# Kernel tuning notes

Hardware: AMD Instinct MI355X
Metric: run time of the kernel (lower is better)

## Reference

```python
import jax, jax.numpy as jnp
from jax import lax
import numpy as np

B, T, F, H = 4096, 512, 8, 16  # batch, seq, n_features, hidden_dim


def _lstm(x, Wih, Whh, bih, bhh):
    """PyTorch-convention LSTM over batch-first x [B,T,in].
    Returns (h_T [B,H], outputs [B,T,H]). Gate order: i, f, g, o."""
    Bn = x.shape[0]
    Hn = Whh.shape[1]
    xs = jnp.swapaxes(x, 0, 1)                       # [T,B,in]
    x_proj = xs @ Wih.T + (bih + bhh)                # precompute input GEMM: [T,B,4H]

    def step(carry, xp):
        h, c = carry
        gates = xp + h @ Whh.T                       # [B,4H]
        i, f, g, o = jnp.split(gates, 4, axis=-1)
        i = jax.nn.sigmoid(i)
        f = jax.nn.sigmoid(f)
        g = jnp.tanh(g)
        o = jax.nn.sigmoid(o)
        c = f * c + i * g
        h = o * jnp.tanh(c)
        return (h, c), h

    h0 = jnp.zeros((Bn, Hn), x.dtype)
    (hT, _), hs = lax.scan(step, (h0, h0), x_proj)
    return hT, jnp.swapaxes(hs, 0, 1)                # [B,H], [B,T,H]


def setup_inputs() -> dict:
    key = jax.random.key(0)
    ks = jax.random.split(key, 11)
    s_e = 1.0 / np.sqrt(H)
    u = lambda k, shp: jax.random.uniform(k, shp, jnp.float32, -s_e, s_e)
    return {
        "x": jax.random.normal(ks[0], (B, T, F), jnp.float32),
        "enc_Wih": u(ks[1], (4 * H, F)),
        "enc_Whh": u(ks[2], (4 * H, H)),
        "enc_bih": u(ks[3], (4 * H,)),
        "enc_bhh": u(ks[4], (4 * H,)),
        "dec_Wih": u(ks[5], (4 * H, H)),
        "dec_Whh": u(ks[6], (4 * H, H)),
        "dec_bih": u(ks[7], (4 * H,)),
        "dec_bhh": u(ks[8], (4 * H,)),
        "out_W": u(ks[9], (F, H)),
        "out_b": u(ks[10], (F,)),
    }


def reference(x, enc_Wih, enc_Whh, enc_bih, enc_bhh,
              dec_Wih, dec_Whh, dec_bih, dec_bhh, out_W, out_b):
    # encoder: keep only final hidden state h_T
    hT, _ = _lstm(x, enc_Wih, enc_Whh, enc_bih, enc_bhh)   # [B,H]
    # repeat over time: h.squeeze(0).unsqueeze(1).repeat(1,T,1)
    repeated = jnp.broadcast_to(hT[:, None, :], (x.shape[0], x.shape[1], hT.shape[1]))
    _, decoded = _lstm(repeated, dec_Wih, dec_Whh, dec_bih, dec_bhh)  # [B,T,H]
    return decoded @ out_W.T + out_b                       # [B,T,F]
```

## Files before the change

### kernel.cpp

```cpp
#include <hip/hip_runtime.h>

#define B_ 4096
#define T_ 512
#define F_ 8
#define H_ 16

typedef float f32x2 __attribute__((ext_vector_type(2)));
typedef float f32x4v __attribute__((ext_vector_type(4)));

__device__ __forceinline__ f32x2 pkfma(f32x2 a, f32x2 b, f32x2 c) {
    return __builtin_elementwise_fma(a, b, c);
}
#define SV2(v, a, b) __builtin_shufflevector(v, v, a, b)

#define LOG2E 1.442695041f
#define N2LOG2E (-2.885390082f)

__device__ __forceinline__ float sigf(float x) {
    return __builtin_amdgcn_rcpf(1.0f + __builtin_amdgcn_exp2f(-LOG2E * x));
}
__device__ __forceinline__ float tanh_f(float x) {
    return __builtin_fmaf(2.0f,
        __builtin_amdgcn_rcpf(1.0f + __builtin_amdgcn_exp2f(N2LOG2E * x)), -1.0f);
}

__global__ __launch_bounds__(256, 1) void lstm_ae_kernel(
    const float* __restrict__ x,
    const float* __restrict__ eWih, const float* __restrict__ eWhh,
    const float* __restrict__ ebih, const float* __restrict__ ebhh,
    const float* __restrict__ dWih, const float* __restrict__ dWhh,
    const float* __restrict__ dbih, const float* __restrict__ dbhh,
    const float* __restrict__ oW,   const float* __restrict__ ob,
    float* __restrict__ out)
{
    const int tid = threadIdx.x;
    const int wv  = tid >> 6;
    const int l   = tid & 63;
    const int cw  = l >> 4;
    const int u   = l & 15;
    const int bw  = blockIdx.x * 16 + wv * 4;
    const int b   = bw + cw;

    __shared__ __align__(16) f32x2 hsh[4][40];
    __shared__ __align__(16) f32x2 xsh[4][4][33][4];

    const f32x2 zero2 = {0.0f, 0.0f};

    f32x2 wh[4][8], wi[4][4];
    float bias[4];
#pragma unroll
    for (int g = 0; g < 4; ++g) {
        const int r = g * 16 + u;
        const f32x2* phh = (const f32x2*)(eWhh + r * 16);
#pragma unroll
        for (int p = 0; p < 8; ++p) wh[g][p] = phh[p];
        const f32x2* pih = (const f32x2*)(eWih + r * 8);
#pragma unroll
        for (int p = 0; p < 4; ++p) wi[g][p] = pih[p];
        bias[g] = ebih[r] + ebhh[r];
    }

    float c = 0.0f;
    f32x2 hb[8];
#pragma unroll
    for (int p = 0; p < 8; ++p) hb[p] = zero2;

    float* hp = (float*)&hsh[wv][cw * 10];

    const int ps = l >> 1, phx = l & 1;
    f32x4v xr[4];
#pragma unroll
    for (int i = 0; i < 4; ++i)
        xr[i] = *(const f32x4v*)(x + ((size_t)(bw + i) * T_ + ps) * F_ + phx * 4);

    for (int c0 = 0; c0 < T_; c0 += 32) {
        __builtin_amdgcn_wave_barrier();
#pragma unroll
        for (int i = 0; i < 4; ++i)
            *(f32x4v*)&xsh[wv][i][ps][phx * 2] = xr[i];
        __builtin_amdgcn_wave_barrier();
        if (c0 + 32 < T_) {
#pragma unroll
            for (int i = 0; i < 4; ++i)
                xr[i] = *(const f32x4v*)(
                    x + ((size_t)(bw + i) * T_ + (c0 + 32 + ps)) * F_ + phx * 4);
        }
        for (int s = 0; s < 32; ++s) {
            f32x4v xq0 = *(const f32x4v*)&xsh[wv][cw][s][0];
            f32x4v xq1 = *(const f32x4v*)&xsh[wv][cw][s][2];
            f32x2 x0 = SV2(xq0, 0, 1), x1 = SV2(xq0, 2, 3);
            f32x2 x2 = SV2(xq1, 0, 1), x3 = SV2(xq1, 2, 3);

            f32x2 acc[4];
#pragma unroll
            for (int g = 0; g < 4; ++g) {
                f32x2 a = pkfma(wi[g][0], x0, f32x2{bias[g], 0.0f});
                a = pkfma(wi[g][1], x1, a);
                a = pkfma(wi[g][2], x2, a);
                a = pkfma(wi[g][3], x3, a);
#pragma unroll
                for (int p = 0; p < 8; ++p) a = pkfma(wh[g][p], hb[p], a);
                acc[g] = a;
            }
            const float gi = sigf(acc[0].x + acc[0].y);
            const float gf = sigf(acc[1].x + acc[1].y);
            const float gg = tanh_f(acc[2].x + acc[2].y);
            const float go = sigf(acc[3].x + acc[3].y);
            c = __builtin_fmaf(gf, c, gi * gg);
            const float ht = go * tanh_f(c);

            __builtin_amdgcn_wave_barrier();
            hp[u] = ht;
            __builtin_amdgcn_wave_barrier();
            f32x4v h0 = *(const f32x4v*)&hp[0];
            f32x4v h1 = *(const f32x4v*)&hp[4];
            f32x4v h2 = *(const f32x4v*)&hp[8];
            f32x4v h3 = *(const f32x4v*)&hp[12];
            hb[0] = SV2(h0, 0, 1); hb[1] = SV2(h0, 2, 3);
            hb[2] = SV2(h1, 0, 1); hb[3] = SV2(h1, 2, 3);
            hb[4] = SV2(h2, 0, 1); hb[5] = SV2(h2, 2, 3);
            hb[6] = SV2(h3, 0, 1); hb[7] = SV2(h3, 2, 3);
        }
    }

    f32x2 wd[4][8];
    float xp[4];
#pragma unroll
    for (int g = 0; g < 4; ++g) {
        const int r = g * 16 + u;
        const f32x2* pih = (const f32x2*)(dWih + r * 16);
        f32x2 a = zero2;
#pragma unroll
        for (int p = 0; p < 8; ++p) a = pkfma(pih[p], hb[p], a);
        xp[g] = dbih[r] + dbhh[r] + a.x + a.y;
        const f32x2* phh = (const f32x2*)(dWhh + r * 16);
#pragma unroll
        for (int p = 0; p < 8; ++p) wd[g][p] = phh[p];
    }
    f32x2 wo[8];
    {
        const f32x2* po = (const f32x2*)(oW + (u & 7) * 16);
#pragma unroll
        for (int p = 0; p < 8; ++p) wo[p] = po[p];
    }
    const float obv = ob[u & 7];
    const bool st = (u < 8);
    float* outp = out + (size_t)b * (T_ * F_);

    c = 0.0f;
#pragma unroll
    for (int p = 0; p < 8; ++p) hb[p] = zero2;

    for (int t = 0; t < T_; ++t) {
        f32x2 acc[4];
#pragma unroll
        for (int g = 0; g < 4; ++g) {
            f32x2 a = pkfma(wd[g][0], hb[0], f32x2{xp[g], 0.0f});
#pragma unroll
            for (int p = 1; p < 8; ++p) a = pkfma(wd[g][p], hb[p], a);
            acc[g] = a;
        }
        const float gi = sigf(acc[0].x + acc[0].y);
        const float gf = sigf(acc[1].x + acc[1].y);
        const float gg = tanh_f(acc[2].x + acc[2].y);
        const float go = sigf(acc[3].x + acc[3].y);
        c = __builtin_fmaf(gf, c, gi * gg);
        const float ht = go * tanh_f(c);

        __builtin_amdgcn_wave_barrier();
        hp[u] = ht;
        __builtin_amdgcn_wave_barrier();
        f32x4v h0 = *(const f32x4v*)&hp[0];
        f32x4v h1 = *(const f32x4v*)&hp[4];
        f32x4v h2 = *(const f32x4v*)&hp[8];
        f32x4v h3 = *(const f32x4v*)&hp[12];
        hb[0] = SV2(h0, 0, 1); hb[1] = SV2(h0, 2, 3);
        hb[2] = SV2(h1, 0, 1); hb[3] = SV2(h1, 2, 3);
        hb[4] = SV2(h2, 0, 1); hb[5] = SV2(h2, 2, 3);
        hb[6] = SV2(h3, 0, 1); hb[7] = SV2(h3, 2, 3);

        f32x2 oa = pkfma(wo[0], hb[0], f32x2{obv, 0.0f});
#pragma unroll
        for (int p = 1; p < 8; ++p) oa = pkfma(wo[p], hb[p], oa);
        if (st) outp[t * F_ + u] = oa.x + oa.y;
    }
}

extern "C" void kernel_launch(void* const* d_in, const int* in_sizes, int n_in,
                              void* d_out, int out_size, void* d_ws, size_t ws_size,
                              hipStream_t stream) {
    (void)in_sizes; (void)n_in; (void)d_ws; (void)ws_size; (void)out_size;
    lstm_ae_kernel<<<dim3(B_ / 16), dim3(256), 0, stream>>>(
        (const float*)d_in[0],
        (const float*)d_in[1], (const float*)d_in[2],
        (const float*)d_in[3], (const float*)d_in[4],
        (const float*)d_in[5], (const float*)d_in[6],
        (const float*)d_in[7], (const float*)d_in[8],
        (const float*)d_in[9], (const float*)d_in[10],
        (float*)d_out);
}
```

Measured before the change: 353.9 us.

## Split LSTM gates across 32 lanes per sequence with swizzle exchange

Moves from 16 lanes per batch element (each computing all four gates) to 32 lanes per element, each computing two gate rows. Gate activations are exchanged with ds_swizzle, and the output projection is split across lanes and reduced with swizzles. This halves the per-lane serial FMA chain on each recurrent step and doubles the grid, with launch bounds raised to allow two blocks per CU. The cost is twice as many lanes per sequence, extra cross-lane swizzles, and idle half-lanes during the h store.

```diff
diff --git a/kernel.cpp b/kernel.cpp
--- a/kernel.cpp
+++ b/kernel.cpp
@@ -23,8 +23,15 @@
     return __builtin_fmaf(2.0f,
         __builtin_amdgcn_rcpf(1.0f + __builtin_amdgcn_exp2f(N2LOG2E * x)), -1.0f);
 }
-
-__global__ __launch_bounds__(256, 1) void lstm_ae_kernel(
+template <int PAT>
+__device__ __forceinline__ float swz(float v) {
+    return __builtin_bit_cast(float,
+        __builtin_amdgcn_ds_swizzle(__builtin_bit_cast(int, v), PAT));
+}
+#define XOR8  0x201F
+#define XOR16 0x401F
+
+__global__ __launch_bounds__(256, 2) void lstm_ae_kernel(
     const float* __restrict__ x,
     const float* __restrict__ eWih, const float* __restrict__ eWhh,
     const float* __restrict__ ebih, const float* __restrict__ ebhh,
@@ -36,82 +43,89 @@
     const int tid = threadIdx.x;
     const int wv  = tid >> 6;
     const int l   = tid & 63;
-    const int cw  = l >> 4;
-    const int u   = l & 15;
-    const int bw  = blockIdx.x * 16 + wv * 4;
-    const int b   = bw + cw;
-
-    __shared__ __align__(16) f32x2 hsh[4][40];
-    __shared__ __align__(16) f32x2 xsh[4][4][33][4];
-
+    const int cw  = l >> 5;
+    const int w   = l & 31;
+    const int u   = w & 15;
+    const bool loh = (w < 16);
+    const int r0  = w;
+    const int r1  = w + 32;
+    const int b   = blockIdx.x * 8 + wv * 2 + cw;
+
+    __shared__ __align__(16) float hsh[4][2][16];
+    __shared__ __align__(16) float xsh[4][2][32][8];
+
+    const float ns1 = loh ? N2LOG2E : -LOG2E;
+    const float m1  = loh ? 2.0f : 1.0f;
+    const float c1  = loh ? -1.0f : 0.0f;
     const f32x2 zero2 = {0.0f, 0.0f};
 
-    f32x2 wh[4][8], wi[4][4];
-    float bias[4];
-#pragma unroll
-    for (int g = 0; g < 4; ++g) {
-        const int r = g * 16 + u;
-        const f32x2* phh = (const f32x2*)(eWhh + r * 16);
-#pragma unroll
-        for (int p = 0; p < 8; ++p) wh[g][p] = phh[p];
-        const f32x2* pih = (const f32x2*)(eWih + r * 8);
-#pragma unroll
-        for (int p = 0; p < 4; ++p) wi[g][p] = pih[p];
-        bias[g] = ebih[r] + ebhh[r];
-    }
+    f32x2 wh0[8], wh1[8], wi0[4], wi1[4];
+    {
+        const f32x2* p0 = (const f32x2*)(eWhh + r0 * 16);
+        const f32x2* p1 = (const f32x2*)(eWhh + r1 * 16);
+#pragma unroll
+        for (int p = 0; p < 8; ++p) { wh0[p] = p0[p]; wh1[p] = p1[p]; }
+        const f32x2* q0 = (const f32x2*)(eWih + r0 * 8);
+        const f32x2* q1 = (const f32x2*)(eWih + r1 * 8);
+#pragma unroll
+        for (int p = 0; p < 4; ++p) { wi0[p] = q0[p]; wi1[p] = q1[p]; }
+    }
+    const float bias0 = ebih[r0] + ebhh[r0];
+    const float bias1 = ebih[r1] + ebhh[r1];
 
     float c = 0.0f;
     f32x2 hb[8];
 #pragma unroll
     for (int p = 0; p < 8; ++p) hb[p] = zero2;
 
-    float* hp = (float*)&hsh[wv][cw * 10];
-
-    const int ps = l >> 1, phx = l & 1;
-    f32x4v xr[4];
-#pragma unroll
-    for (int i = 0; i < 4; ++i)
-        xr[i] = *(const f32x4v*)(x + ((size_t)(bw + i) * T_ + ps) * F_ + phx * 4);
+    const int sA = w >> 1, hA = (w & 1) * 4;
+    const float* xbase = x + (size_t)b * (T_ * F_);
+    f32x4v xrA = *(const f32x4v*)(xbase + sA * F_ + hA);
+    f32x4v xrB = *(const f32x4v*)(xbase + (sA + 16) * F_ + hA);
 
     for (int c0 = 0; c0 < T_; c0 += 32) {
         __builtin_amdgcn_wave_barrier();
-#pragma unroll
-        for (int i = 0; i < 4; ++i)
-            *(f32x4v*)&xsh[wv][i][ps][phx * 2] = xr[i];
+        *(f32x4v*)&xsh[wv][cw][sA][hA]      = xrA;
+        *(f32x4v*)&xsh[wv][cw][sA + 16][hA] = xrB;
         __builtin_amdgcn_wave_barrier();
         if (c0 + 32 < T_) {
-#pragma unroll
-            for (int i = 0; i < 4; ++i)
-                xr[i] = *(const f32x4v*)(
-                    x + ((size_t)(bw + i) * T_ + (c0 + 32 + ps)) * F_ + phx * 4);
+            xrA = *(const f32x4v*)(xbase + (c0 + 32 + sA) * F_ + hA);
+            xrB = *(const f32x4v*)(xbase + (c0 + 48 + sA) * F_ + hA);
         }
         for (int s = 0; s < 32; ++s) {
             f32x4v xq0 = *(const f32x4v*)&xsh[wv][cw][s][0];
-            f32x4v xq1 = *(const f32x4v*)&xsh[wv][cw][s][2];
+            f32x4v xq1 = *(const f32x4v*)&xsh[wv][cw][s][4];
             f32x2 x0 = SV2(xq0, 0, 1), x1 = SV2(xq0, 2, 3);
             f32x2 x2 = SV2(xq1, 0, 1), x3 = SV2(xq1, 2, 3);
 
-            f32x2 acc[4];
-#pragma unroll
-            for (int g = 0; g < 4; ++g) {
-                f32x2 a = pkfma(wi[g][0], x0, f32x2{bias[g], 0.0f});
-                a = pkfma(wi[g][1], x1, a);
-                a = pkfma(wi[g][2], x2, a);
-                a = pkfma(wi[g][3], x3, a);
-#pragma unroll
-                for (int p = 0; p < 8; ++p) a = pkfma(wh[g][p], hb[p], a);
-                acc[g] = a;
+            f32x2 aa0 = pkfma(wi0[0], x0, f32x2{bias0, 0.0f});
+            f32x2 ab0 = pkfma(wi0[1], x1, zero2);
+            f32x2 aa1 = pkfma(wi1[0], x0, f32x2{bias1, 0.0f});
+            f32x2 ab1 = pkfma(wi1[1], x1, zero2);
+            aa0 = pkfma(wi0[2], x2, aa0); ab0 = pkfma(wi0[3], x3, ab0);
+            aa1 = pkfma(wi1[2], x2, aa1); ab1 = pkfma(wi1[3], x3, ab1);
+#pragma unroll
+            for (int p = 0; p < 8; p += 2) {
+                aa0 = pkfma(wh0[p],   hb[p],   aa0);
+                ab0 = pkfma(wh0[p+1], hb[p+1], ab0);
+                aa1 = pkfma(wh1[p],   hb[p],   aa1);
+                ab1 = pkfma(wh1[p+1], hb[p+1], ab1);
             }
-            const float gi = sigf(acc[0].x + acc[0].y);
-            const float gf = sigf(acc[1].x + acc[1].y);
-            const float gg = tanh_f(acc[2].x + acc[2].y);
-            const float go = sigf(acc[3].x + acc[3].y);
-            c = __builtin_fmaf(gf, c, gi * gg);
-            const float ht = go * tanh_f(c);
+            f32x2 t0 = aa0 + ab0; const float s0 = t0.x + t0.y;
+            f32x2 t1 = aa1 + ab1; const float s1 = t1.x + t1.y;
+
+            const float a0 = sigf(s0);
+            const float a1 = __builtin_fmaf(
+                m1, __builtin_amdgcn_rcpf(1.0f + __builtin_amdgcn_exp2f(ns1 * s1)), c1);
+            const float e0 = swz<XOR16>(a0);
+            const float e1 = swz<XOR16>(a1);
+            c = __builtin_fmaf(e0, c, a0 * a1);
+            const float ht = e1 * tanh_f(c);
 
             __builtin_amdgcn_wave_barrier();
-            hp[u] = ht;
+            if (loh) hsh[wv][cw][u] = ht;
             __builtin_amdgcn_wave_barrier();
+            const float* hp = &hsh[wv][cw][0];
             f32x4v h0 = *(const f32x4v*)&hp[0];
             f32x4v h1 = *(const f32x4v*)&hp[4];
             f32x4v h2 = *(const f32x4v*)&hp[8];
@@ -123,28 +137,29 @@
         }
     }
 
-    f32x2 wd[4][8];
-    float xp[4];
-#pragma unroll
-    for (int g = 0; g < 4; ++g) {
-        const int r = g * 16 + u;
-        const f32x2* pih = (const f32x2*)(dWih + r * 16);
-        f32x2 a = zero2;
-#pragma unroll
-        for (int p = 0; p < 8; ++p) a = pkfma(pih[p], hb[p], a);
-        xp[g] = dbih[r] + dbhh[r] + a.x + a.y;
-        const f32x2* phh = (const f32x2*)(dWhh + r * 16);
-#pragma unroll
-        for (int p = 0; p < 8; ++p) wd[g][p] = phh[p];
-    }
-    f32x2 wo[8];
+    f32x2 wd0[8], wd1[8];
+    float xp0, xp1;
     {
-        const f32x2* po = (const f32x2*)(oW + (u & 7) * 16);
-#pragma unroll
-        for (int p = 0; p < 8; ++p) wo[p] = po[p];
-    }
-    const float obv = ob[u & 7];
-    const bool st = (u < 8);
+        const f32x2* pi0 = (const f32x2*)(dWih + r0 * 16);
+        const f32x2* pi1 = (const f32x2*)(dWih + r1 * 16);
+        f32x2 a0 = zero2, a1 = zero2;
+#pragma unroll
+        for (int p = 0; p < 8; ++p) {
+            a0 = pkfma(pi0[p], hb[p], a0);
+            a1 = pkfma(pi1[p], hb[p], a1);
+        }
+        xp0 = dbih[r0] + dbhh[r0] + a0.x + a0.y;
+        xp1 = dbih[r1] + dbhh[r1] + a1.x + a1.y;
+        const f32x2* ph0 = (const f32x2*)(dWhh + r0 * 16);
+        const f32x2* ph1 = (const f32x2*)(dWhh + r1 * 16);
+#pragma unroll
+        for (int p = 0; p < 8; ++p) { wd0[p] = ph0[p]; wd1[p] = ph1[p]; }
+    }
+    const int fo = w & 7, kq = w >> 3;
+    f32x2 wo0 = ((const f32x2*)(oW + fo * 16))[kq * 2 + 0];
+    f32x2 wo1 = ((const f32x2*)(oW + fo * 16))[kq * 2 + 1];
+    const float obv = ob[fo];
+    const bool st = (w < 8);
     float* outp = out + (size_t)b * (T_ * F_);
 
     c = 0.0f;
@@ -152,24 +167,32 @@
     for (int p = 0; p < 8; ++p) hb[p] = zero2;
 
     for (int t = 0; t < T_; ++t) {
-        f32x2 acc[4];
-#pragma unroll
-        for (int g = 0; g < 4; ++g) {
-            f32x2 a = pkfma(wd[g][0], hb[0], f32x2{xp[g], 0.0f});
-#pragma unroll
-            for (int p = 1; p < 8; ++p) a = pkfma(wd[g][p], hb[p], a);
-            acc[g] = a;
-        }
-        const float gi = sigf(acc[0].x + acc[0].y);
-        const float gf = sigf(acc[1].x + acc[1].y);
-        const float gg = tanh_f(acc[2].x + acc[2].y);
-        const float go = sigf(acc[3].x + acc[3].y);
-        c = __builtin_fmaf(gf, c, gi * gg);
-        const float ht = go * tanh_f(c);
-
-        __builtin_amdgcn_wave_barrier();
-        hp[u] = ht;
-        __builtin_amdgcn_wave_barrier();
+        f32x2 aa0 = pkfma(wd0[0], hb[0], f32x2{xp0, 0.0f});
+        f32x2 ab0 = pkfma(wd0[1], hb[1], zero2);
+        f32x2 aa1 = pkfma(wd1[0], hb[0], f32x2{xp1, 0.0f});
+        f32x2 ab1 = pkfma(wd1[1], hb[1], zero2);
+#pragma unroll
+        for (int p = 2; p < 8; p += 2) {
+            aa0 = pkfma(wd0[p],   hb[p],   aa0);
+            ab0 = pkfma(wd0[p+1], hb[p+1], ab0);
+            aa1 = pkfma(wd1[p],   hb[p],   aa1);
+            ab1 = pkfma(wd1[p+1], hb[p+1], ab1);
+        }
+        f32x2 t0 = aa0 + ab0; const float s0 = t0.x + t0.y;
+        f32x2 t1 = aa1 + ab1; const float s1 = t1.x + t1.y;
+
+        const float a0 = sigf(s0);
+        const float a1 = __builtin_fmaf(
+            m1, __builtin_amdgcn_rcpf(1.0f + __builtin_amdgcn_exp2f(ns1 * s1)), c1);
+        const float e0 = swz<XOR16>(a0);
+        const float e1 = swz<XOR16>(a1);
+        c = __builtin_fmaf(e0, c, a0 * a1);
+        const float ht = e1 * tanh_f(c);
+
+        __builtin_amdgcn_wave_barrier();
+        if (loh) hsh[wv][cw][u] = ht;
+        __builtin_amdgcn_wave_barrier();
+        const float* hp = &hsh[wv][cw][0];
         f32x4v h0 = *(const f32x4v*)&hp[0];
         f32x4v h1 = *(const f32x4v*)&hp[4];
         f32x4v h2 = *(const f32x4v*)&hp[8];
@@ -179,10 +202,12 @@
         hb[4] = SV2(h2, 0, 1); hb[5] = SV2(h2, 2, 3);
         hb[6] = SV2(h3, 0, 1); hb[7] = SV2(h3, 2, 3);
 
-        f32x2 oa = pkfma(wo[0], hb[0], f32x2{obv, 0.0f});
-#pragma unroll
-        for (int p = 1; p < 8; ++p) oa = pkfma(wo[p], hb[p], oa);
-        if (st) outp[t * F_ + u] = oa.x + oa.y;
+        f32x2 oa = pkfma(wo0, hb[kq * 2], zero2);
+        oa = pkfma(wo1, hb[kq * 2 + 1], oa);
+        float os = oa.x + oa.y;
+        os += swz<XOR8>(os);
+        os += swz<XOR16>(os);
+        if (st) outp[t * F_ + w] = os + obv;
     }
 }
 
@@ -190,7 +215,7 @@
                               void* d_out, int out_size, void* d_ws, size_t ws_size,
                               hipStream_t stream) {
     (void)in_sizes; (void)n_in; (void)d_ws; (void)ws_size; (void)out_size;
-    lstm_ae_kernel<<<dim3(B_ / 16), dim3(256), 0, stream>>>(
+    lstm_ae_kernel<<<dim3(B_ / 8), dim3(256), 0, stream>>>(
         (const float*)d_in[0],
         (const float*)d_in[1], (const float*)d_in[2],
         (const float*)d_in[3], (const float*)d_in[4],
```

New measurement: 614.5 us. 73.6% more time.

## Broadcast LSTM hidden state via DPP row rotations instead of LDS round-trip

Applied to the files above, without the earlier changes.

Replaces the per-step LDS write/read of the 16-element hidden vector with 15 DPP row_ror moves, so each lane gets all hidden values rotated within its 16-lane row. Recurrent and output weights are pre-permuted to match the rotation order. The dot products change from packed f32x2 FMAs to scalar FMAs with two accumulators. This removes LDS latency and wave barriers from the serial recurrence, at the cost of more VALU instructions per step, since scalar FMAs replace packed ones and the DPP moves are added.

```diff
diff --git a/kernel.cpp b/kernel.cpp
--- a/kernel.cpp
+++ b/kernel.cpp
@@ -24,6 +24,21 @@
         __builtin_amdgcn_rcpf(1.0f + __builtin_amdgcn_exp2f(N2LOG2E * x)), -1.0f);
 }
 
+template <int K>
+__device__ __forceinline__ float rotr(float v) {
+    int i = __builtin_bit_cast(int, v);
+    return __builtin_bit_cast(float,
+        __builtin_amdgcn_update_dpp(i, i, 0x120 + K, 0xF, 0xF, false));
+}
+__device__ __forceinline__ void rot_all(float ht, float* hr) {
+    hr[0]  = ht;
+    hr[1]  = rotr<1>(ht);  hr[2]  = rotr<2>(ht);  hr[3]  = rotr<3>(ht);
+    hr[4]  = rotr<4>(ht);  hr[5]  = rotr<5>(ht);  hr[6]  = rotr<6>(ht);
+    hr[7]  = rotr<7>(ht);  hr[8]  = rotr<8>(ht);  hr[9]  = rotr<9>(ht);
+    hr[10] = rotr<10>(ht); hr[11] = rotr<11>(ht); hr[12] = rotr<12>(ht);
+    hr[13] = rotr<13>(ht); hr[14] = rotr<14>(ht); hr[15] = rotr<15>(ht);
+}
+
 __global__ __launch_bounds__(256, 1) void lstm_ae_kernel(
     const float* __restrict__ x,
     const float* __restrict__ eWih, const float* __restrict__ eWhh,
@@ -41,19 +56,19 @@
     const int bw  = blockIdx.x * 16 + wv * 4;
     const int b   = bw + cw;
 
-    __shared__ __align__(16) f32x2 hsh[4][40];
     __shared__ __align__(16) f32x2 xsh[4][4][33][4];
 
     const f32x2 zero2 = {0.0f, 0.0f};
 
-    f32x2 wh[4][8], wi[4][4];
+    float wr[4][16];
+    f32x2 wi[4][4];
     float bias[4];
 #pragma unroll
     for (int g = 0; g < 4; ++g) {
         const int r = g * 16 + u;
-        const f32x2* phh = (const f32x2*)(eWhh + r * 16);
 #pragma unroll
-        for (int p = 0; p < 8; ++p) wh[g][p] = phh[p];
+        for (int k = 0; k < 16; ++k)
+            wr[g][k] = eWhh[r * 16 + ((u - k) & 15)];
         const f32x2* pih = (const f32x2*)(eWih + r * 8);
 #pragma unroll
         for (int p = 0; p < 4; ++p) wi[g][p] = pih[p];
@@ -61,11 +76,9 @@
     }
 
     float c = 0.0f;
-    f32x2 hb[8];
+    float hrot[16];
 #pragma unroll
-    for (int p = 0; p < 8; ++p) hb[p] = zero2;
-
-    float* hp = (float*)&hsh[wv][cw * 10];
+    for (int k = 0; k < 16; ++k) hrot[k] = 0.0f;
 
     const int ps = l >> 1, phx = l & 1;
     f32x4v xr[4];
@@ -91,98 +104,82 @@
             f32x2 x0 = SV2(xq0, 0, 1), x1 = SV2(xq0, 2, 3);
             f32x2 x2 = SV2(xq1, 0, 1), x3 = SV2(xq1, 2, 3);
 
-            f32x2 acc[4];
+            float sg[4];
 #pragma unroll
             for (int g = 0; g < 4; ++g) {
-                f32x2 a = pkfma(wi[g][0], x0, f32x2{bias[g], 0.0f});
-                a = pkfma(wi[g][1], x1, a);
-                a = pkfma(wi[g][2], x2, a);
-                a = pkfma(wi[g][3], x3, a);
+                f32x2 pa = pkfma(wi[g][0], x0, f32x2{bias[g], 0.0f});
+                f32x2 pb = pkfma(wi[g][1], x1, zero2);
+                pa = pkfma(wi[g][2], x2, pa);
+                pb = pkfma(wi[g][3], x3, pb);
+                f32x2 ts = pa + pb;
+                float cA = ts.x + ts.y, cB = 0.0f;
 #pragma unroll
-                for (int p = 0; p < 8; ++p) a = pkfma(wh[g][p], hb[p], a);
-                acc[g] = a;
+                for (int k = 0; k < 16; k += 2) {
+                    cA = __builtin_fmaf(wr[g][k],     hrot[k],     cA);
+                    cB = __builtin_fmaf(wr[g][k + 1], hrot[k + 1], cB);
+                }
+                sg[g] = cA + cB;
             }
-            const float gi = sigf(acc[0].x + acc[0].y);
-            const float gf = sigf(acc[1].x + acc[1].y);
-            const float gg = tanh_f(acc[2].x + acc[2].y);
-            const float go = sigf(acc[3].x + acc[3].y);
+            const float gi = sigf(sg[0]);
+            const float gf = sigf(sg[1]);
+            const float gg = tanh_f(sg[2]);
+            const float go = sigf(sg[3]);
             c = __builtin_fmaf(gf, c, gi * gg);
             const float ht = go * tanh_f(c);
-
-            __builtin_amdgcn_wave_barrier();
-            hp[u] = ht;
-            __builtin_amdgcn_wave_barrier();
-            f32x4v h0 = *(const f32x4v*)&hp[0];
-            f32x4v h1 = *(const f32x4v*)&hp[4];
-            f32x4v h2 = *(const f32x4v*)&hp[8];
-            f32x4v h3 = *(const f32x4v*)&hp[12];
-            hb[0] = SV2(h0, 0, 1); hb[1] = SV2(h0, 2, 3);
-            hb[2] = SV2(h1, 0, 1); hb[3] = SV2(h1, 2, 3);
-            hb[4] = SV2(h2, 0, 1); hb[5] = SV2(h2, 2, 3);
-            hb[6] = SV2(h3, 0, 1); hb[7] = SV2(h3, 2, 3);
+            rot_all(ht, hrot);
         }
     }
 
-    f32x2 wd[4][8];
-    float xp[4];
+    float wd[4][16], wo[16], xp[4];
 #pragma unroll
     for (int g = 0; g < 4; ++g) {
         const int r = g * 16 + u;
-        const f32x2* pih = (const f32x2*)(dWih + r * 16);
-        f32x2 a = zero2;
+        float a = 0.0f;
 #pragma unroll
-        for (int p = 0; p < 8; ++p) a = pkfma(pih[p], hb[p], a);
-        xp[g] = dbih[r] + dbhh[r] + a.x + a.y;
-        const f32x2* phh = (const f32x2*)(dWhh + r * 16);
+        for (int k = 0; k < 16; ++k) {
+            wd[g][k] = dWhh[r * 16 + ((u - k) & 15)];
+            a = __builtin_fmaf(dWih[r * 16 + ((u - k) & 15)], hrot[k], a);
+        }
+        xp[g] = dbih[r] + dbhh[r] + a;
+    }
 #pragma unroll
-        for (int p = 0; p < 8; ++p) wd[g][p] = phh[p];
-    }
-    f32x2 wo[8];
-    {
-        const f32x2* po = (const f32x2*)(oW + (u & 7) * 16);
-#pragma unroll
-        for (int p = 0; p < 8; ++p) wo[p] = po[p];
-    }
+    for (int k = 0; k < 16; ++k)
+        wo[k] = oW[(u & 7) * 16 + ((u - k) & 15)];
     const float obv = ob[u & 7];
     const bool st = (u < 8);
     float* outp = out + (size_t)b * (T_ * F_);
 
     c = 0.0f;
 #pragma unroll
-    for (int p = 0; p < 8; ++p) hb[p] = zero2;
+    for (int k = 0; k < 16; ++k) hrot[k] = 0.0f;
 
     for (int t = 0; t < T_; ++t) {
-        f32x2 acc[4];
+        float sg[4];
 #pragma unroll
         for (int g = 0; g < 4; ++g) {
-            f32x2 a = pkfma(wd[g][0], hb[0], f32x2{xp[g], 0.0f});
+            float cA = xp[g], cB = 0.0f;
 #pragma unroll
-            for (int p = 1; p < 8; ++p) a = pkfma(wd[g][p], hb[p], a);
-            acc[g] = a;
+            for (int k = 0; k < 16; k += 2) {
+                cA = __builtin_fmaf(wd[g][k],     hrot[k],     cA);
+                cB = __builtin_fmaf(wd[g][k + 1], hrot[k + 1], cB);
+            }
+            sg[g] = cA + cB;
         }
-        const float gi = sigf(acc[0].x + acc[0].y);
-        const float gf = sigf(acc[1].x + acc[1].y);
-        const float gg = tanh_f(acc[2].x + acc[2].y);
-        const float go = sigf(acc[3].x + acc[3].y);
+        const float gi = sigf(sg[0]);
+        const float gf = sigf(sg[1]);
+        const float gg = tanh_f(sg[2]);
+        const float go = sigf(sg[3]);
         c = __builtin_fmaf(gf, c, gi * gg);
         const float ht = go * tanh_f(c);
+        rot_all(ht, hrot);
 
-        __builtin_amdgcn_wave_barrier();
-        hp[u] = ht;
-        __builtin_amdgcn_wave_barrier();
-        f32x4v h0 = *(const f32x4v*)&hp[0];
-        f32x4v h1 = *(const f32x4v*)&hp[4];
-        f32x4v h2 = *(const f32x4v*)&hp[8];
-        f32x4v h3 = *(const f32x4v*)&hp[12];
-        hb[0] = SV2(h0, 0, 1); hb[1] = SV2(h0, 2, 3);
-        hb[2] = SV2(h1, 0, 1); hb[3] = SV2(h1, 2, 3);
-        hb[4] = SV2(h2, 0, 1); hb[5] = SV2(h2, 2, 3);
-        hb[6] = SV2(h3, 0, 1); hb[7] = SV2(h3, 2, 3);
-
-        f32x2 oa = pkfma(wo[0], hb[0], f32x2{obv, 0.0f});
+        float oA = obv, oB = 0.0f;
 #pragma unroll
-        for (int p = 1; p < 8; ++p) oa = pkfma(wo[p], hb[p], oa);
-        if (st) outp[t * F_ + u] = oa.x + oa.y;
+        for (int k = 0; k < 16; k += 2) {
+            oA = __builtin_fmaf(wo[k],     hrot[k],     oA);
+            oB = __builtin_fmaf(wo[k + 1], hrot[k + 1], oB);
+        }
+        if (st) outp[t * F_ + u] = oA + oB;
     }
 }
 
```

Result: slower. 406.6 us (+14.9%).

## Shorten LSTM step critical path via split accumulators and overlapped input/output projections

Applied to the files above, without the earlier changes.

Each gate's dot product is split into two independent packed-FMA accumulator chains that are summed at the end, roughly halving the serial FMA depth per timestep. The encoder's input projection for step s+1 is computed inside the window between the LDS write and read of h, so only the recurrent FMAs stay on the critical path. The decoder's output projection for step t-1 is deferred into that same window, with a tail computation after the loop. This targets latency in the strictly sequential recurrence, at the cost of extra live registers and a slightly different floating-point summation order.

```diff
diff --git a/kernel.cpp b/kernel.cpp
--- a/kernel.cpp
+++ b/kernel.cpp
@@ -46,8 +46,7 @@
 
     const f32x2 zero2 = {0.0f, 0.0f};
 
-    f32x2 wh[4][8], wi[4][4];
-    float bias[4];
+    f32x2 wh[4][8], wi[4][4], bias2[4];
 #pragma unroll
     for (int g = 0; g < 4; ++g) {
         const int r = g * 16 + u;
@@ -57,7 +56,7 @@
         const f32x2* pih = (const f32x2*)(eWih + r * 8);
 #pragma unroll
         for (int p = 0; p < 4; ++p) wi[g][p] = pih[p];
-        bias[g] = ebih[r] + ebhh[r];
+        bias2[g] = f32x2{ebih[r] + ebhh[r], 0.0f};
     }
 
     float c = 0.0f;
@@ -72,6 +71,8 @@
 #pragma unroll
     for (int i = 0; i < 4; ++i)
         xr[i] = *(const f32x4v*)(x + ((size_t)(bw + i) * T_ + ps) * F_ + phx * 4);
+
+    f32x2 xaA[4], xaB[4];
 
     for (int c0 = 0; c0 < T_; c0 += 32) {
         __builtin_amdgcn_wave_barrier();
@@ -85,32 +86,55 @@
                 xr[i] = *(const f32x4v*)(
                     x + ((size_t)(bw + i) * T_ + (c0 + 32 + ps)) * F_ + phx * 4);
         }
+        {
+            f32x4v q0 = *(const f32x4v*)&xsh[wv][cw][0][0];
+            f32x4v q1 = *(const f32x4v*)&xsh[wv][cw][0][2];
+            f32x2 x0 = SV2(q0, 0, 1), x1 = SV2(q0, 2, 3);
+            f32x2 x2 = SV2(q1, 0, 1), x3 = SV2(q1, 2, 3);
+#pragma unroll
+            for (int g = 0; g < 4; ++g) {
+                f32x2 a = pkfma(wi[g][0], x0, bias2[g]);
+                f32x2 bq = pkfma(wi[g][1], x1, zero2);
+                xaA[g] = pkfma(wi[g][2], x2, a);
+                xaB[g] = pkfma(wi[g][3], x3, bq);
+            }
+        }
         for (int s = 0; s < 32; ++s) {
-            f32x4v xq0 = *(const f32x4v*)&xsh[wv][cw][s][0];
-            f32x4v xq1 = *(const f32x4v*)&xsh[wv][cw][s][2];
-            f32x2 x0 = SV2(xq0, 0, 1), x1 = SV2(xq0, 2, 3);
-            f32x2 x2 = SV2(xq1, 0, 1), x3 = SV2(xq1, 2, 3);
-
-            f32x2 acc[4];
+            float sg[4];
 #pragma unroll
             for (int g = 0; g < 4; ++g) {
-                f32x2 a = pkfma(wi[g][0], x0, f32x2{bias[g], 0.0f});
-                a = pkfma(wi[g][1], x1, a);
-                a = pkfma(wi[g][2], x2, a);
-                a = pkfma(wi[g][3], x3, a);
-#pragma unroll
-                for (int p = 0; p < 8; ++p) a = pkfma(wh[g][p], hb[p], a);
-                acc[g] = a;
-            }
-            const float gi = sigf(acc[0].x + acc[0].y);
-            const float gf = sigf(acc[1].x + acc[1].y);
-            const float gg = tanh_f(acc[2].x + acc[2].y);
-            const float go = sigf(acc[3].x + acc[3].y);
+                f32x2 aa = xaA[g], ab = xaB[g];
+#pragma unroll
+                for (int p = 0; p < 8; p += 2) {
+                    aa = pkfma(wh[g][p],   hb[p],   aa);
+                    ab = pkfma(wh[g][p+1], hb[p+1], ab);
+                }
+                f32x2 ts = aa + ab;
+                sg[g] = ts.x + ts.y;
+            }
+            const float gi = sigf(sg[0]);
+            const float gf = sigf(sg[1]);
+            const float gg = tanh_f(sg[2]);
+            const float go = sigf(sg[3]);
             c = __builtin_fmaf(gf, c, gi * gg);
             const float ht = go * tanh_f(c);
 
             __builtin_amdgcn_wave_barrier();
             hp[u] = ht;
+            __builtin_amdgcn_wave_barrier();
+            {
+                f32x4v q0 = *(const f32x4v*)&xsh[wv][cw][s + 1][0];
+                f32x4v q1 = *(const f32x4v*)&xsh[wv][cw][s + 1][2];
+                f32x2 x0 = SV2(q0, 0, 1), x1 = SV2(q0, 2, 3);
+                f32x2 x2 = SV2(q1, 0, 1), x3 = SV2(q1, 2, 3);
+#pragma unroll
+                for (int g = 0; g < 4; ++g) {
+                    f32x2 a = pkfma(wi[g][0], x0, bias2[g]);
+                    f32x2 bq = pkfma(wi[g][1], x1, zero2);
+                    xaA[g] = pkfma(wi[g][2], x2, a);
+                    xaB[g] = pkfma(wi[g][3], x3, bq);
+                }
+            }
             __builtin_amdgcn_wave_barrier();
             f32x4v h0 = *(const f32x4v*)&hp[0];
             f32x4v h1 = *(const f32x4v*)&hp[4];
@@ -123,8 +147,7 @@
         }
     }
 
-    f32x2 wd[4][8];
-    float xp[4];
+    f32x2 wd[4][8], xp2[4];
 #pragma unroll
     for (int g = 0; g < 4; ++g) {
         const int r = g * 16 + u;
@@ -132,7 +155,7 @@
         f32x2 a = zero2;
 #pragma unroll
         for (int p = 0; p < 8; ++p) a = pkfma(pih[p], hb[p], a);
-        xp[g] = dbih[r] + dbhh[r] + a.x + a.y;
+        xp2[g] = f32x2{dbih[r] + dbhh[r] + a.x + a.y, 0.0f};
         const f32x2* phh = (const f32x2*)(dWhh + r * 16);
 #pragma unroll
         for (int p = 0; p < 8; ++p) wd[g][p] = phh[p];
@@ -143,7 +166,7 @@
 #pragma unroll
         for (int p = 0; p < 8; ++p) wo[p] = po[p];
     }
-    const float obv = ob[u & 7];
+    const f32x2 ob2 = {ob[u & 7], 0.0f};
     const bool st = (u < 8);
     float* outp = out + (size_t)b * (T_ * F_);
 
@@ -152,23 +175,40 @@
     for (int p = 0; p < 8; ++p) hb[p] = zero2;
 
     for (int t = 0; t < T_; ++t) {
-        f32x2 acc[4];
+        float sg[4];
 #pragma unroll
         for (int g = 0; g < 4; ++g) {
-            f32x2 a = pkfma(wd[g][0], hb[0], f32x2{xp[g], 0.0f});
-#pragma unroll
-            for (int p = 1; p < 8; ++p) a = pkfma(wd[g][p], hb[p], a);
-            acc[g] = a;
-        }
-        const float gi = sigf(acc[0].x + acc[0].y);
-        const float gf = sigf(acc[1].x + acc[1].y);
-        const float gg = tanh_f(acc[2].x + acc[2].y);
-        const float go = sigf(acc[3].x + acc[3].y);
+            f32x2 aa = pkfma(wd[g][0], hb[0], xp2[g]);
+            f32x2 ab = pkfma(wd[g][1], hb[1], zero2);
+#pragma unroll
+            for (int p = 2; p < 8; p += 2) {
+                aa = pkfma(wd[g][p],   hb[p],   aa);
+                ab = pkfma(wd[g][p+1], hb[p+1], ab);
+            }
+            f32x2 ts = aa + ab;
+            sg[g] = ts.x + ts.y;
+        }
+        const float gi = sigf(sg[0]);
+        const float gf = sigf(sg[1]);
+        const float gg = tanh_f(sg[2]);
+        const float go = sigf(sg[3]);
         c = __builtin_fmaf(gf, c, gi * gg);
         const float ht = go * tanh_f(c);
 
         __builtin_amdgcn_wave_barrier();
         hp[u] = ht;
+        __builtin_amdgcn_wave_barrier();
+        {
+            f32x2 oa  = pkfma(wo[0], hb[0], ob2);
+            f32x2 obb = pkfma(wo[1], hb[1], zero2);
+#pragma unroll
+            for (int p = 2; p < 8; p += 2) {
+                oa  = pkfma(wo[p],   hb[p],   oa);
+                obb = pkfma(wo[p+1], hb[p+1], obb);
+            }
+            f32x2 to = oa + obb;
+            if (st && t > 0) outp[(t - 1) * F_ + u] = to.x + to.y;
+        }
         __builtin_amdgcn_wave_barrier();
         f32x4v h0 = *(const f32x4v*)&hp[0];
         f32x4v h1 = *(const f32x4v*)&hp[4];
@@ -178,11 +218,17 @@
         hb[2] = SV2(h1, 0, 1); hb[3] = SV2(h1, 2, 3);
         hb[4] = SV2(h2, 0, 1); hb[5] = SV2(h2, 2, 3);
         hb[6] = SV2(h3, 0, 1); hb[7] = SV2(h3, 2, 3);
-
-        f32x2 oa = pkfma(wo[0], hb[0], f32x2{obv, 0.0f});
-#pragma unroll
-        for (int p = 1; p < 8; ++p) oa = pkfma(wo[p], hb[p], oa);
-        if (st) outp[t * F_ + u] = oa.x + oa.y;
+    }
+    {
+        f32x2 oa  = pkfma(wo[0], hb[0], ob2);
+        f32x2 obb = pkfma(wo[1], hb[1], zero2);
+#pragma unroll
+        for (int p = 2; p < 8; p += 2) {
+            oa  = pkfma(wo[p],   hb[p],   oa);
+            obb = pkfma(wo[p+1], hb[p+1], obb);
+        }
+        f32x2 to = oa + obb;
+        if (st) outp[(T_ - 1) * F_ + u] = to.x + to.y;
     }
 }
 
```

After: 364.1 us. +2.9%, slower.
